# Kernel optimization log

Hardware: AMD Instinct MI355X
Metric: run time of the kernel (lower is better)

The kernel has to match this reference:

```python
import jax, jax.numpy as jnp
import numpy as np

NEG_INF = -1e30  # stand-in for float('-inf') that is safe under softmax


def setup_inputs() -> dict:
    key = jax.random.key(0)
    k1, k2, k3, k4 = jax.random.split(key, 4)
    B, T, C, H = 4, 4096, 1024, 128
    x = jax.random.normal(k1, (B, T, C), dtype=jnp.float32)
    # nn.Linear(n_emb, head_size, bias=False): store as [C, H] so y = x @ W
    Wk = jax.random.normal(k2, (C, H), dtype=jnp.float32) * (C ** -0.5)
    Wq = jax.random.normal(k3, (C, H), dtype=jnp.float32) * (C ** -0.5)
    Wv = jax.random.normal(k4, (C, H), dtype=jnp.float32) * (C ** -0.5)
    return {"x": x, "Wk": Wk, "Wq": Wq, "Wv": Wv}


def reference(x, Wk, Wq, Wv):
    B, T, C = x.shape
    k = x @ Wk  # [B, T, H]
    q = x @ Wq  # [B, T, H]
    v = x @ Wv  # [B, T, H]
    # Faithful to original: wei = k @ q^T, scaled by C**-0.5 (C = n_emb)
    wei = jnp.einsum('bih,bjh->bij', k, q) * (C ** -0.5)  # [B, T, T]
    causal = jnp.tril(jnp.ones((T, T), dtype=bool))
    wei = jnp.where(causal, wei, NEG_INF)
    wei = jax.nn.softmax(wei, axis=-1)
    out = jnp.einsum('bij,bjh->bih', wei, v)  # [B, T, H]
    return out
```

## Files before the change

### kernel.cpp

```cpp
#include <hip/hip_runtime.h>
#include <hip/hip_bf16.h>

#define T_SEQ 4096
#define NBATCH 4
#define C_EMB 1024
#define H_DIM 128
#define M_ROWS (NBATCH * T_SEQ)
#define SPLIT 4

typedef __bf16 bf16x8 __attribute__((ext_vector_type(8)));
typedef float  floatx4 __attribute__((ext_vector_type(4)));

__device__ __forceinline__ ushort f2bf(float f) {
    __hip_bfloat16 h = __float2bfloat16(f);
    return *reinterpret_cast<ushort*>(&h);
}
__device__ __forceinline__ float bf2f(ushort u) {
    unsigned int v = ((unsigned int)u) << 16;
    return *reinterpret_cast<float*>(&v);
}
__device__ __forceinline__ uint4 pack8(const float4& a, const float4& b) {
    __hip_bfloat162 h0 = __float22bfloat162_rn(make_float2(a.x, a.y));
    __hip_bfloat162 h1 = __float22bfloat162_rn(make_float2(a.z, a.w));
    __hip_bfloat162 h2 = __float22bfloat162_rn(make_float2(b.x, b.y));
    __hip_bfloat162 h3 = __float22bfloat162_rn(make_float2(b.z, b.w));
    uint4 r;
    r.x = *reinterpret_cast<unsigned int*>(&h0);
    r.y = *reinterpret_cast<unsigned int*>(&h1);
    r.z = *reinterpret_cast<unsigned int*>(&h2);
    r.w = *reinterpret_cast<unsigned int*>(&h3);
    return r;
}
__device__ __forceinline__ void gld16(const ushort* g, ushort* l) {
    __builtin_amdgcn_global_load_lds(
        (const __attribute__((address_space(1))) unsigned int*)(g),
        (__attribute__((address_space(3))) unsigned int*)(l),
        16, 0, 0);
}

__global__ __launch_bounds__(256) void transpose_w(
    const float* __restrict__ Wk, const float* __restrict__ Wq,
    const float* __restrict__ Wv, ushort* __restrict__ wt) {
    const int z = blockIdx.y;
    const float* W = (z == 0) ? Wk : (z == 1) ? Wq : Wv;
    ushort* Wtz = wt + (size_t)z * H_DIM * C_EMB;
    int linear = blockIdx.x * 256 + threadIdx.x;
    int n  = linear >> 9;
    int k0 = (linear & 511) << 1;
    float a = W[(size_t)k0 * H_DIM + n];
    float b = W[(size_t)(k0 + 1) * H_DIM + n];
    ushort2 o;
    o.x = f2bf(a);
    o.y = f2bf(b);
    *reinterpret_cast<ushort2*>(Wtz + (size_t)n * C_EMB + k0) = o;
}

__global__ __launch_bounds__(256, 2) void qkv_gemm(
    const float* __restrict__ x, const ushort* __restrict__ wt,
    ushort* __restrict__ kqv) {
    const int m0 = blockIdx.x * 32;

    __shared__ ushort As[2][32 * 32];
    __shared__ ushort Bs[2][384 * 32];

    const int tid  = threadIdx.x;
    const int lane = tid & 63;
    const int wave = tid >> 6;
    const int l15  = lane & 15;
    const int quad = lane >> 4;

    floatx4 acc[2][6];
#pragma unroll
    for (int mi = 0; mi < 2; ++mi)
#pragma unroll
        for (int ni = 0; ni < 6; ++ni)
            acc[mi][ni] = floatx4{0.f, 0.f, 0.f, 0.f};

    auto stageB = [&](int kt, int buf) {
#pragma unroll
        for (int i = 0; i < 6; ++i) {
            int row = wave * 96 + i * 16 + (lane >> 2);
            int chg = (lane & 3) ^ (row & 3);
            gld16(wt + (size_t)row * C_EMB + kt * 32 + chg * 8,
                  Bs[buf] + (wave * 96 + i * 16) * 32);
        }
    };

    stageB(0, 0);
    if (tid < 128) {
        int r = tid >> 2, ch = tid & 3;
        const float* src = x + (size_t)(m0 + r) * C_EMB + ch * 8;
        float4 v0 = *reinterpret_cast<const float4*>(src);
        float4 v1 = *reinterpret_cast<const float4*>(src + 4);
        *reinterpret_cast<uint4*>(As[0] + r * 32 + ((ch ^ (r & 3))) * 8) = pack8(v0, v1);
    }

    for (int kt = 0; kt < 32; ++kt) {
        const int buf = kt & 1;
        __syncthreads();
        float4 xa0, xa1;
        int r = tid >> 2, ch = tid & 3;
        if (kt + 1 < 32) {
            stageB(kt + 1, buf ^ 1);
            if (tid < 128) {
                const float* src = x + (size_t)(m0 + r) * C_EMB + (kt + 1) * 32 + ch * 8;
                xa0 = *reinterpret_cast<const float4*>(src);
                xa1 = *reinterpret_cast<const float4*>(src + 4);
            }
        }
        bf16x8 a[2];
#pragma unroll
        for (int mi = 0; mi < 2; ++mi)
            a[mi] = *reinterpret_cast<const bf16x8*>(
                As[buf] + (mi * 16 + l15) * 32 + (quad ^ (l15 & 3)) * 8);
#pragma unroll
        for (int ni = 0; ni < 6; ++ni) {
            bf16x8 b = *reinterpret_cast<const bf16x8*>(
                Bs[buf] + (wave * 96 + ni * 16 + l15) * 32 + (quad ^ (l15 & 3)) * 8);
#pragma unroll
            for (int mi = 0; mi < 2; ++mi)
                acc[mi][ni] = __builtin_amdgcn_mfma_f32_16x16x32_bf16(a[mi], b, acc[mi][ni], 0, 0, 0);
        }
        if (kt + 1 < 32 && tid < 128) {
            *reinterpret_cast<uint4*>(As[buf ^ 1] + r * 32 + ((ch ^ (r & 3))) * 8) = pack8(xa0, xa1);
        }
    }

    ushort* vt = kqv + (size_t)2 * M_ROWS * H_DIM;
#pragma unroll
    for (int ni = 0; ni < 6; ++ni) {
        const int ng = wave * 96 + ni * 16;
        const int z  = ng >> 7;
        const int nz = (ng & 127) + l15;
        if (z < 2) {
            const float scale = (z == 0) ? 0.03125f : 1.0f;
            ushort* outz = kqv + (size_t)z * M_ROWS * H_DIM;
#pragma unroll
            for (int mi = 0; mi < 2; ++mi)
#pragma unroll
                for (int r = 0; r < 4; ++r) {
                    int row = m0 + mi * 16 + quad * 4 + r;
                    outz[(size_t)row * H_DIM + nz] = f2bf(acc[mi][ni][r] * scale);
                }
        } else {
#pragma unroll
            for (int mi = 0; mi < 2; ++mi) {
                int trow = m0 + mi * 16 + quad * 4;
                int bb   = trow >> 12;
                int tloc = trow & (T_SEQ - 1);
                ushort4 pk;
                pk.x = f2bf(acc[mi][ni][0]);
                pk.y = f2bf(acc[mi][ni][1]);
                pk.z = f2bf(acc[mi][ni][2]);
                pk.w = f2bf(acc[mi][ni][3]);
                *reinterpret_cast<ushort4*>(
                    vt + ((size_t)(bb * H_DIM + nz) << 12) + tloc) = pk;
            }
        }
    }
}

#define P_STRIDE 72
__global__ __launch_bounds__(256, 3) void flash_chunk(
    const ushort* __restrict__ kqv, ushort* __restrict__ partO,
    float* __restrict__ partL) {
    const int it = 63 - (blockIdx.x >> 2);
    const int c  = blockIdx.x & 3;
    if (c > it) return;
    const int b  = blockIdx.y;
    const int i0 = it * 64;

    const ushort* Qg = kqv + (size_t)b * T_SEQ * H_DIM;
    const ushort* Kg = kqv + (size_t)M_ROWS * H_DIM + (size_t)b * T_SEQ * H_DIM;
    const ushort* Vt = kqv + (size_t)2 * M_ROWS * H_DIM + (size_t)b * H_DIM * T_SEQ;

    __shared__ ushort Ks[64 * 128];
    __shared__ ushort Vs[128 * 64];
    __shared__ ushort Ps[4][16 * P_STRIDE];

    const int tid  = threadIdx.x;
    const int lane = tid & 63;
    const int wave = tid >> 6;
    const int l15  = lane & 15;
    const int quad = lane >> 4;

    bf16x8 q[4];
    {
        const ushort* qrow = Qg + (size_t)(i0 + wave * 16 + l15) * H_DIM + quad * 8;
#pragma unroll
        for (int kk = 0; kk < 4; ++kk)
            q[kk] = *reinterpret_cast<const bf16x8*>(qrow + kk * 32);
    }

    float l_i[4] = {0.f, 0.f, 0.f, 0.f};
    floatx4 o[8];
#pragma unroll
    for (int nh = 0; nh < 8; ++nh) o[nh] = floatx4{0.f, 0.f, 0.f, 0.f};

    ushort* Pw = Ps[wave];

    for (int jt = c; jt <= it; jt += SPLIT) {
        const int j0 = jt * 64;
        __syncthreads();
#pragma unroll
        for (int i = 0; i < 4; ++i) {
            int row = wave * 16 + i * 4 + (lane >> 4);
            int chg = (lane & 15) ^ (row & 15);
            gld16(Kg + (size_t)(j0 + row) * H_DIM + chg * 8,
                  Ks + (wave * 16 + i * 4) * 128);
        }
#pragma unroll
        for (int i = 0; i < 4; ++i) {
            int row = wave * 32 + i * 8 + (lane >> 3);
            int chg = (lane & 7) ^ (row & 7);
            gld16(Vt + (size_t)row * T_SEQ + j0 + chg * 8,
                  Vs + (wave * 32 + i * 8) * 64);
        }
        __syncthreads();

        floatx4 s[4];
#pragma unroll
        for (int ni = 0; ni < 4; ++ni) s[ni] = floatx4{0.f, 0.f, 0.f, 0.f};
#pragma unroll
        for (int kk = 0; kk < 4; ++kk)
#pragma unroll
            for (int ni = 0; ni < 4; ++ni) {
                bf16x8 kb = *reinterpret_cast<const bf16x8*>(
                    Ks + (ni * 16 + l15) * 128 + ((4 * kk + quad) ^ l15) * 8);
                s[ni] = __builtin_amdgcn_mfma_f32_16x16x32_bf16(q[kk], kb, s[ni], 0, 0, 0);
            }

        if (jt == it) {
            int ii = i0 + wave * 16 + quad * 4;
#pragma unroll
            for (int ni = 0; ni < 4; ++ni) {
                int j = j0 + ni * 16 + l15;
#pragma unroll
                for (int r = 0; r < 4; ++r)
                    if (j > ii + r) s[ni][r] = -1e30f;
            }
        }

#pragma unroll
        for (int ni = 0; ni < 4; ++ni)
#pragma unroll
            for (int r = 0; r < 4; ++r) {
                float p = __expf(s[ni][r]);
                l_i[r] += p;
                Pw[(quad * 4 + r) * P_STRIDE + ni * 16 + l15] = f2bf(p);
            }

#pragma unroll
        for (int kp = 0; kp < 2; ++kp) {
            bf16x8 a = *reinterpret_cast<const bf16x8*>(
                Pw + l15 * P_STRIDE + kp * 32 + quad * 8);
#pragma unroll
            for (int nh = 0; nh < 8; ++nh) {
                bf16x8 vb = *reinterpret_cast<const bf16x8*>(
                    Vs + (nh * 16 + l15) * 64 + ((4 * kp + quad) ^ (l15 & 7)) * 8);
                o[nh] = __builtin_amdgcn_mfma_f32_16x16x32_bf16(a, vb, o[nh], 0, 0, 0);
            }
        }
    }

#pragma unroll
    for (int r = 0; r < 4; ++r) {
        float v = l_i[r];
#pragma unroll
        for (int off = 8; off >= 1; off >>= 1)
            v += __shfl_xor(v, off, 64);
        l_i[r] = v;
    }

    const int idx = ((b * 64 + it) << 2) + c;
    ushort* po = partO + (size_t)idx * 64 * 128;
#pragma unroll
    for (int nh = 0; nh < 8; ++nh)
#pragma unroll
        for (int r = 0; r < 4; ++r) {
            int row = wave * 16 + quad * 4 + r;
            po[(size_t)row * 128 + nh * 16 + l15] = f2bf(o[nh][r]);
        }
    if (l15 == 0) {
        float* ml = partL + (size_t)idx * 64;
#pragma unroll
        for (int r = 0; r < 4; ++r)
            ml[wave * 16 + quad * 4 + r] = l_i[r];
    }
}

__global__ __launch_bounds__(256) void combine(
    const ushort* __restrict__ partO, const float* __restrict__ partL,
    float* __restrict__ out) {
    const int it   = blockIdx.x >> 1;
    const int half = blockIdx.x & 1;
    const int b    = blockIdx.y;
    const int count = min(SPLIT, it + 1);
    const int tid  = threadIdx.x;
    const int base = (b * 64 + it) << 2;

    __shared__ float invLs[32];
    if (tid < 32) {
        int row = half * 32 + tid;
        float L = 0.f;
        for (int cc = 0; cc < count; ++cc)
            L += partL[(size_t)(base + cc) * 64 + row];
        invLs[tid] = 1.0f / L;
    }
    __syncthreads();

    float* outb = out + ((size_t)b * T_SEQ + it * 64 + half * 32) * H_DIM;
#pragma unroll
    for (int rep = 0; rep < 4; ++rep) {
        int idx = rep * 256 + tid;
        int row = idx >> 5;
        int cg  = (idx & 31) * 4;
        float4 acc = make_float4(0.f, 0.f, 0.f, 0.f);
        for (int cc = 0; cc < count; ++cc) {
            ushort4 p = *reinterpret_cast<const ushort4*>(
                partO + (size_t)(base + cc) * 8192 + (size_t)(half * 32 + row) * 128 + cg);
            acc.x += bf2f(p.x);
            acc.y += bf2f(p.y);
            acc.z += bf2f(p.z);
            acc.w += bf2f(p.w);
        }
        float invL = invLs[row];
        acc.x *= invL; acc.y *= invL; acc.z *= invL; acc.w *= invL;
        *reinterpret_cast<float4*>(outb + (size_t)row * H_DIM + cg) = acc;
    }
}

extern "C" void kernel_launch(void* const* d_in, const int* in_sizes, int n_in,
                              void* d_out, int out_size, void* d_ws, size_t ws_size,
                              hipStream_t stream) {
    const float* x  = (const float*)d_in[0];
    const float* Wk = (const float*)d_in[1];
    const float* Wq = (const float*)d_in[2];
    const float* Wv = (const float*)d_in[3];

    ushort* kqv   = (ushort*)d_ws;
    ushort* wt    = kqv + (size_t)3 * M_ROWS * H_DIM;
    ushort* partO = wt + (size_t)3 * H_DIM * C_EMB;
    float*  partL = (float*)(partO + (size_t)1024 * 64 * 128);

    transpose_w<<<dim3(256, 3), 256, 0, stream>>>(Wk, Wq, Wv, wt);
    qkv_gemm<<<dim3(512), 256, 0, stream>>>(x, wt, kqv);
    flash_chunk<<<dim3(64 * SPLIT, NBATCH), 256, 0, stream>>>(kqv, partO, partL);
    combine<<<dim3(128, NBATCH), 256, 0, stream>>>(partO, partL, (float*)d_out);
}
```

Before: 183.9 us.

## Fuse split-K combine into flash kernel and rewrite QKV GEMM without LDS

Removes the separate combine kernel. Each flash_chunk block bumps an atomic counter per query tile, and the last finishing split reduces the partial outputs and writes the final result. The counters are reset inside the weight-transpose kernel. The QKV projection is also rewritten to load x and weight fragments straight from global memory into registers and use 32x32x16 MFMA, with register double-buffering instead of LDS staging and barriers. This saves a kernel launch and LDS sync overhead, but risks uncoalesced, redundant global loads in the GEMM and serialized tail work in the last block per tile.

```diff
diff --git a/kernel.cpp b/kernel.cpp
--- a/kernel.cpp
+++ b/kernel.cpp
@@ -8,8 +8,9 @@
 #define M_ROWS (NBATCH * T_SEQ)
 #define SPLIT 4
 
-typedef __bf16 bf16x8 __attribute__((ext_vector_type(8)));
-typedef float  floatx4 __attribute__((ext_vector_type(4)));
+typedef __bf16 bf16x8  __attribute__((ext_vector_type(8)));
+typedef float  floatx4  __attribute__((ext_vector_type(4)));
+typedef float  floatx16 __attribute__((ext_vector_type(16)));
 
 __device__ __forceinline__ ushort f2bf(float f) {
     __hip_bfloat16 h = __float2bfloat16(f);
@@ -40,7 +41,10 @@
 
 __global__ __launch_bounds__(256) void transpose_w(
     const float* __restrict__ Wk, const float* __restrict__ Wq,
-    const float* __restrict__ Wv, ushort* __restrict__ wt) {
+    const float* __restrict__ Wv, ushort* __restrict__ wt,
+    int* __restrict__ done) {
+    if (blockIdx.x == 0 && blockIdx.y == 0)
+        done[threadIdx.x] = 0;
     const int z = blockIdx.y;
     const float* W = (z == 0) ? Wk : (z == 1) ? Wq : Wv;
     ushort* Wtz = wt + (size_t)z * H_DIM * C_EMB;
@@ -55,13 +59,114 @@
     *reinterpret_cast<ushort2*>(Wtz + (size_t)n * C_EMB + k0) = o;
 }
 
-__global__ __launch_bounds__(256, 2) void qkv_gemm(
+struct GFrags {
+    float4 a[2][2];
+    uint4  b[2][3];
+};
+
+__global__ __launch_bounds__(256) void qkv_gemm(
     const float* __restrict__ x, const ushort* __restrict__ wt,
     ushort* __restrict__ kqv) {
-    const int m0 = blockIdx.x * 32;
-
-    __shared__ ushort As[2][32 * 32];
-    __shared__ ushort Bs[2][384 * 32];
+    const int m0   = blockIdx.x * 32;
+    const int tid  = threadIdx.x;
+    const int lane = tid & 63;
+    const int wave = tid >> 6;
+    const int l31  = lane & 31;
+    const int half = lane >> 5;
+
+    const float*  xp = x  + (size_t)(m0 + l31) * C_EMB + half * 8;
+    const ushort* wp = wt + (size_t)(wave * 96 + l31) * C_EMB + half * 8;
+
+    floatx16 acc[3];
+#pragma unroll
+    for (int ni = 0; ni < 3; ++ni)
+#pragma unroll
+        for (int r = 0; r < 16; ++r) acc[ni][r] = 0.f;
+
+    auto loadF = [&](int kt, GFrags& f) {
+#pragma unroll
+        for (int s = 0; s < 2; ++s) {
+            const float* ap = xp + kt * 32 + s * 16;
+            f.a[s][0] = *reinterpret_cast<const float4*>(ap);
+            f.a[s][1] = *reinterpret_cast<const float4*>(ap + 4);
+#pragma unroll
+            for (int ni = 0; ni < 3; ++ni)
+                f.b[s][ni] = *reinterpret_cast<const uint4*>(
+                    wp + (size_t)ni * 32 * C_EMB + kt * 32 + s * 16);
+        }
+    };
+    auto compF = [&](GFrags& f) {
+#pragma unroll
+        for (int s = 0; s < 2; ++s) {
+            uint4 ua = pack8(f.a[s][0], f.a[s][1]);
+            bf16x8 av = *reinterpret_cast<bf16x8*>(&ua);
+#pragma unroll
+            for (int ni = 0; ni < 3; ++ni) {
+                bf16x8 bv = *reinterpret_cast<bf16x8*>(&f.b[s][ni]);
+                acc[ni] = __builtin_amdgcn_mfma_f32_32x32x16_bf16(av, bv, acc[ni], 0, 0, 0);
+            }
+        }
+    };
+
+    GFrags fA, fB;
+    loadF(0, fA);
+    for (int kt = 0; kt < 32; kt += 2) {
+        loadF(kt + 1, fB);
+        compF(fA);
+        if (kt + 2 < 32) loadF(kt + 2, fA);
+        compF(fB);
+    }
+
+    ushort* vt = kqv + (size_t)2 * M_ROWS * H_DIM;
+#pragma unroll
+    for (int ni = 0; ni < 3; ++ni) {
+        const int ng = wave * 96 + ni * 32;
+        const int z  = ng >> 7;
+        const int nz = (ng & 127) + l31;
+        if (z < 2) {
+            const float scale = (z == 0) ? 0.03125f : 1.0f;
+            ushort* outz = kqv + (size_t)z * M_ROWS * H_DIM;
+#pragma unroll
+            for (int r = 0; r < 16; ++r) {
+                int row = m0 + (r & 3) + 8 * (r >> 2) + 4 * half;
+                outz[(size_t)row * H_DIM + nz] = f2bf(acc[ni][r] * scale);
+            }
+        } else {
+#pragma unroll
+            for (int g = 0; g < 4; ++g) {
+                int trow = m0 + 8 * g + 4 * half;
+                int bb   = trow >> 12;
+                int tloc = trow & (T_SEQ - 1);
+                ushort4 pk;
+                pk.x = f2bf(acc[ni][4 * g + 0]);
+                pk.y = f2bf(acc[ni][4 * g + 1]);
+                pk.z = f2bf(acc[ni][4 * g + 2]);
+                pk.w = f2bf(acc[ni][4 * g + 3]);
+                *reinterpret_cast<ushort4*>(
+                    vt + ((size_t)(bb * H_DIM + nz) << 12) + tloc) = pk;
+            }
+        }
+    }
+}
+
+#define P_STRIDE 72
+__global__ __launch_bounds__(256, 3) void flash_chunk(
+    const ushort* __restrict__ kqv, ushort* __restrict__ partO,
+    float* __restrict__ partL, int* __restrict__ done,
+    float* __restrict__ out) {
+    const int it = 63 - (blockIdx.x >> 2);
+    const int c  = blockIdx.x & 3;
+    if (c > it) return;
+    const int b  = blockIdx.y;
+    const int i0 = it * 64;
+
+    const ushort* Qg = kqv + (size_t)b * T_SEQ * H_DIM;
+    const ushort* Kg = kqv + (size_t)M_ROWS * H_DIM + (size_t)b * T_SEQ * H_DIM;
+    const ushort* Vt = kqv + (size_t)2 * M_ROWS * H_DIM + (size_t)b * H_DIM * T_SEQ;
+
+    __shared__ ushort Ks[64 * 128];
+    __shared__ ushort Vs[128 * 64];
+    __shared__ ushort Ps[4][16 * P_STRIDE];
 
     const int tid  = threadIdx.x;
     const int lane = tid & 63;
@@ -69,121 +174,6 @@
     const int l15  = lane & 15;
     const int quad = lane >> 4;
 
-    floatx4 acc[2][6];
-#pragma unroll
-    for (int mi = 0; mi < 2; ++mi)
-#pragma unroll
-        for (int ni = 0; ni < 6; ++ni)
-            acc[mi][ni] = floatx4{0.f, 0.f, 0.f, 0.f};
-
-    auto stageB = [&](int kt, int buf) {
-#pragma unroll
-        for (int i = 0; i < 6; ++i) {
-            int row = wave * 96 + i * 16 + (lane >> 2);
-            int chg = (lane & 3) ^ (row & 3);
-            gld16(wt + (size_t)row * C_EMB + kt * 32 + chg * 8,
-                  Bs[buf] + (wave * 96 + i * 16) * 32);
-        }
-    };
-
-    stageB(0, 0);
-    if (tid < 128) {
-        int r = tid >> 2, ch = tid & 3;
-        const float* src = x + (size_t)(m0 + r) * C_EMB + ch * 8;
-        float4 v0 = *reinterpret_cast<const float4*>(src);
-        float4 v1 = *reinterpret_cast<const float4*>(src + 4);
-        *reinterpret_cast<uint4*>(As[0] + r * 32 + ((ch ^ (r & 3))) * 8) = pack8(v0, v1);
-    }
-
-    for (int kt = 0; kt < 32; ++kt) {
-        const int buf = kt & 1;
-        __syncthreads();
-        float4 xa0, xa1;
-        int r = tid >> 2, ch = tid & 3;
-        if (kt + 1 < 32) {
-            stageB(kt + 1, buf ^ 1);
-            if (tid < 128) {
-                const float* src = x + (size_t)(m0 + r) * C_EMB + (kt + 1) * 32 + ch * 8;
-                xa0 = *reinterpret_cast<const float4*>(src);
-                xa1 = *reinterpret_cast<const float4*>(src + 4);
-            }
-        }
-        bf16x8 a[2];
-#pragma unroll
-        for (int mi = 0; mi < 2; ++mi)
-            a[mi] = *reinterpret_cast<const bf16x8*>(
-                As[buf] + (mi * 16 + l15) * 32 + (quad ^ (l15 & 3)) * 8);
-#pragma unroll
-        for (int ni = 0; ni < 6; ++ni) {
-            bf16x8 b = *reinterpret_cast<const bf16x8*>(
-                Bs[buf] + (wave * 96 + ni * 16 + l15) * 32 + (quad ^ (l15 & 3)) * 8);
-#pragma unroll
-            for (int mi = 0; mi < 2; ++mi)
-                acc[mi][ni] = __builtin_amdgcn_mfma_f32_16x16x32_bf16(a[mi], b, acc[mi][ni], 0, 0, 0);
-        }
-        if (kt + 1 < 32 && tid < 128) {
-            *reinterpret_cast<uint4*>(As[buf ^ 1] + r * 32 + ((ch ^ (r & 3))) * 8) = pack8(xa0, xa1);
-        }
-    }
-
-    ushort* vt = kqv + (size_t)2 * M_ROWS * H_DIM;
-#pragma unroll
-    for (int ni = 0; ni < 6; ++ni) {
-        const int ng = wave * 96 + ni * 16;
-        const int z  = ng >> 7;
-        const int nz = (ng & 127) + l15;
-        if (z < 2) {
-            const float scale = (z == 0) ? 0.03125f : 1.0f;
-            ushort* outz = kqv + (size_t)z * M_ROWS * H_DIM;
-#pragma unroll
-            for (int mi = 0; mi < 2; ++mi)
-#pragma unroll
-                for (int r = 0; r < 4; ++r) {
-                    int row = m0 + mi * 16 + quad * 4 + r;
-                    outz[(size_t)row * H_DIM + nz] = f2bf(acc[mi][ni][r] * scale);
-                }
-        } else {
-#pragma unroll
-            for (int mi = 0; mi < 2; ++mi) {
-                int trow = m0 + mi * 16 + quad * 4;
-                int bb   = trow >> 12;
-                int tloc = trow & (T_SEQ - 1);
-                ushort4 pk;
-                pk.x = f2bf(acc[mi][ni][0]);
-                pk.y = f2bf(acc[mi][ni][1]);
-                pk.z = f2bf(acc[mi][ni][2]);
-                pk.w = f2bf(acc[mi][ni][3]);
-                *reinterpret_cast<ushort4*>(
-                    vt + ((size_t)(bb * H_DIM + nz) << 12) + tloc) = pk;
-            }
-        }
-    }
-}
-
-#define P_STRIDE 72
-__global__ __launch_bounds__(256, 3) void flash_chunk(
-    const ushort* __restrict__ kqv, ushort* __restrict__ partO,
-    float* __restrict__ partL) {
-    const int it = 63 - (blockIdx.x >> 2);
-    const int c  = blockIdx.x & 3;
-    if (c > it) return;
-    const int b  = blockIdx.y;
-    const int i0 = it * 64;
-
-    const ushort* Qg = kqv + (size_t)b * T_SEQ * H_DIM;
-    const ushort* Kg = kqv + (size_t)M_ROWS * H_DIM + (size_t)b * T_SEQ * H_DIM;
-    const ushort* Vt = kqv + (size_t)2 * M_ROWS * H_DIM + (size_t)b * H_DIM * T_SEQ;
-
-    __shared__ ushort Ks[64 * 128];
-    __shared__ ushort Vs[128 * 64];
-    __shared__ ushort Ps[4][16 * P_STRIDE];
-
-    const int tid  = threadIdx.x;
-    const int lane = tid & 63;
-    const int wave = tid >> 6;
-    const int l15  = lane & 15;
-    const int quad = lane >> 4;
-
     bf16x8 q[4];
     {
         const ushort* qrow = Qg + (size_t)(i0 + wave * 16 + l15) * H_DIM + quad * 8;
@@ -272,7 +262,8 @@
         l_i[r] = v;
     }
 
-    const int idx = ((b * 64 + it) << 2) + c;
+    const int base = (b * 64 + it) << 2;
+    const int idx  = base + c;
     ushort* po = partO + (size_t)idx * 64 * 128;
 #pragma unroll
     for (int nh = 0; nh < 8; ++nh)
@@ -287,38 +278,35 @@
         for (int r = 0; r < 4; ++r)
             ml[wave * 16 + quad * 4 + r] = l_i[r];
     }
-}
-
-__global__ __launch_bounds__(256) void combine(
-    const ushort* __restrict__ partO, const float* __restrict__ partL,
-    float* __restrict__ out) {
-    const int it   = blockIdx.x >> 1;
-    const int half = blockIdx.x & 1;
-    const int b    = blockIdx.y;
+
+    __threadfence();
+    __syncthreads();
+    __shared__ int sOld;
+    if (tid == 0) sOld = atomicAdd(&done[b * 64 + it], 1);
+    __syncthreads();
     const int count = min(SPLIT, it + 1);
-    const int tid  = threadIdx.x;
-    const int base = (b * 64 + it) << 2;
-
-    __shared__ float invLs[32];
-    if (tid < 32) {
-        int row = half * 32 + tid;
+    if (sOld != count - 1) return;
+    __threadfence();
+
+    __shared__ float invLs[64];
+    if (tid < 64) {
         float L = 0.f;
         for (int cc = 0; cc < count; ++cc)
-            L += partL[(size_t)(base + cc) * 64 + row];
+            L += partL[(size_t)(base + cc) * 64 + tid];
         invLs[tid] = 1.0f / L;
     }
     __syncthreads();
 
-    float* outb = out + ((size_t)b * T_SEQ + it * 64 + half * 32) * H_DIM;
-#pragma unroll
-    for (int rep = 0; rep < 4; ++rep) {
-        int idx = rep * 256 + tid;
-        int row = idx >> 5;
-        int cg  = (idx & 31) * 4;
+    float* outb = out + ((size_t)b * T_SEQ + i0) * H_DIM;
+#pragma unroll
+    for (int rep = 0; rep < 8; ++rep) {
+        int id2 = rep * 256 + tid;
+        int row = id2 >> 5;
+        int cg  = (id2 & 31) * 4;
         float4 acc = make_float4(0.f, 0.f, 0.f, 0.f);
         for (int cc = 0; cc < count; ++cc) {
             ushort4 p = *reinterpret_cast<const ushort4*>(
-                partO + (size_t)(base + cc) * 8192 + (size_t)(half * 32 + row) * 128 + cg);
+                partO + (size_t)(base + cc) * 8192 + (size_t)row * 128 + cg);
             acc.x += bf2f(p.x);
             acc.y += bf2f(p.y);
             acc.z += bf2f(p.z);
@@ -342,9 +330,10 @@
     ushort* wt    = kqv + (size_t)3 * M_ROWS * H_DIM;
     ushort* partO = wt + (size_t)3 * H_DIM * C_EMB;
     float*  partL = (float*)(partO + (size_t)1024 * 64 * 128);
-
-    transpose_w<<<dim3(256, 3), 256, 0, stream>>>(Wk, Wq, Wv, wt);
+    int*    done  = (int*)(partL + (size_t)1024 * 64);
+
+    transpose_w<<<dim3(256, 3), 256, 0, stream>>>(Wk, Wq, Wv, wt, done);
     qkv_gemm<<<dim3(512), 256, 0, stream>>>(x, wt, kqv);
-    flash_chunk<<<dim3(64 * SPLIT, NBATCH), 256, 0, stream>>>(kqv, partO, partL);
-    combine<<<dim3(128, NBATCH), 256, 0, stream>>>(partO, partL, (float*)d_out);
-}
+    flash_chunk<<<dim3(64 * SPLIT, NBATCH), 256, 0, stream>>>(
+        kqv, partO, partL, done, (float*)d_out);
+}
```

Result: slower. 484.4 us (+163.4%).
